# Optimization experiments

Measured on AMD Instinct MI355X. Metric: run time of the kernel, lower is better.

## Reference

```python
import jax, jax.numpy as jnp
import numpy as np

B, T, D = 2, 2048, 2048
N_HEADS, N_KV, HEAD_DIM = 8, 4, 256
S_CACHE = 2048
WINDOW = 512
SOFT_CAP = 50.0
ROPE_TS = 10000
ROPE_PROP = 1.0
EPS = 1e-6
NEG_INF = -2.3819763e38


def setup_inputs() -> dict:
    key = jax.random.key(0)
    ks = jax.random.split(key, 6)
    x = jax.random.normal(ks[0], (B, T, D), dtype=jnp.float32)
    wq = jax.random.normal(ks[1], (D, N_HEADS * HEAD_DIM), dtype=jnp.float32) * (D ** -0.5)
    wk = jax.random.normal(ks[2], (D, N_KV * HEAD_DIM), dtype=jnp.float32) * (D ** -0.5)
    wv = jax.random.normal(ks[3], (D, N_KV * HEAD_DIM), dtype=jnp.float32) * (D ** -0.5)
    wo = jax.random.normal(ks[4], (N_HEADS * HEAD_DIM, D), dtype=jnp.float32) * ((N_HEADS * HEAD_DIM) ** -0.5)
    return {
        'x': x,
        'segment_pos': jnp.broadcast_to(jnp.arange(T, dtype=jnp.int32), (B, T)),
        'cur_ind': 0,
        'wq': wq, 'wk': wk, 'wv': wv, 'wo': wo,
        'q_norm_scale': jnp.zeros((HEAD_DIM,), jnp.float32),
        'k_norm_scale': jnp.zeros((HEAD_DIM,), jnp.float32),
        'k_cache': jnp.zeros((B, S_CACHE, N_KV, HEAD_DIM), jnp.float32),
        'v_cache': jnp.zeros((B, S_CACHE, N_KV, HEAD_DIM), jnp.float32),
    }


def _rms_norm(x, scale, eps=EPS):
    # Gemma4RMSNorm: fp32 norm, (1 + scale) offset
    xf = x.astype(jnp.float32)
    n = xf * jax.lax.rsqrt(jnp.mean(jnp.square(xf), -1, keepdims=True) + eps)
    return (n * (1.0 + scale)).astype(x.dtype)


def _apply_rope(x, pos, max_timescale=ROPE_TS, proportion=ROPE_PROP):
    # x: [B, T, n, H]; pos: [B, T]. Partial RoPE on first proportion*H dims.
    H = x.shape[-1]
    rope_dim = int(H * proportion)
    half = rope_dim // 2
    frac = jnp.arange(half, dtype=jnp.float32) / half
    timescale = jnp.asarray(max_timescale, jnp.float32) ** frac  # [half]
    sinusoid = pos.astype(jnp.float32)[..., None] / timescale    # [B, T, half]
    sin = jnp.sin(sinusoid)[:, :, None, :]
    cos = jnp.cos(sinusoid)[:, :, None, :]
    x_rope, x_pass = x[..., :rope_dim], x[..., rope_dim:]
    x1, x2 = x_rope[..., :half], x_rope[..., half:]
    rotated = jnp.concatenate([x1 * cos - x2 * sin, x2 * cos + x1 * sin], axis=-1)
    return jnp.concatenate([rotated, x_pass], axis=-1).astype(x.dtype)


def reference(x, segment_pos, cur_ind, wq, wk, wv, wo, q_norm_scale, k_norm_scale, k_cache, v_cache):
    b, t, _ = x.shape
    g = N_HEADS // N_KV  # GQA group size

    q = (x @ wq).reshape(b, t, N_HEADS, HEAD_DIM)
    k = (x @ wk).reshape(b, t, N_KV, HEAD_DIM)
    v = (x @ wv).reshape(b, t, N_KV, HEAD_DIM)

    # QK-norm (per-head RMSNorm) then RoPE
    q = _rms_norm(q, q_norm_scale)
    k = _rms_norm(k, k_norm_scale)
    q = _apply_rope(q, segment_pos)
    k = _apply_rope(k, segment_pos)

    # KV-cache scatter write at cur_ind
    idx = jnp.asarray(cur_ind, jnp.int32)
    k_cache = jax.lax.dynamic_update_slice(k_cache, k, (0, idx, 0, 0))
    v_cache = jax.lax.dynamic_update_slice(v_cache, v, (0, idx, 0, 0))

    # Attention logits over full cache: [b, kv, g, t, s]
    qg = q.reshape(b, t, N_KV, g, HEAD_DIM) * (HEAD_DIM ** -0.5)
    logits = jnp.einsum('btkgh,bskh->bkgts', qg, k_cache)
    logits = SOFT_CAP * jnp.tanh(logits / SOFT_CAP)

    # Causal + sliding-window mask from absolute positions
    q_pos = segment_pos[:, :, None]                              # [b, t, 1]
    k_pos = jnp.arange(S_CACHE, dtype=jnp.int32)[None, None, :]  # [1, 1, s]
    mask = (k_pos <= q_pos) & (q_pos - k_pos < WINDOW)           # [b, t, s]
    logits = jnp.where(mask[:, None, None, :, :], logits, NEG_INF)

    probs = jax.nn.softmax(logits, axis=-1)
    attn = jnp.einsum('bkgts,bskh->btkgh', probs, v_cache).reshape(b, t, N_HEADS * HEAD_DIM)
    return attn @ wo
```

## Files before the change

kernel.cpp:

```cpp
#include <hip/hip_runtime.h>

#define T_SEQ 2048
#define NHEADS 8
#define NKV 4
#define HD 256
#define WIN 512

typedef __bf16 bf16x8 __attribute__((ext_vector_type(8)));
typedef float f32x4 __attribute__((ext_vector_type(4)));

__device__ __forceinline__ float bf2f(unsigned short u) {
    return __uint_as_float(((unsigned int)u) << 16);
}
__device__ __forceinline__ unsigned short f2bf(float f) {
    unsigned int u = __float_as_uint(f);
    u += 0x7fffu + ((u >> 16) & 1u);
    return (unsigned short)(u >> 16);
}

#define GLOAD_LDS16(gptr, lptr)                                            \
    __builtin_amdgcn_global_load_lds(                                      \
        (const __attribute__((address_space(1))) unsigned int*)(gptr),     \
        (__attribute__((address_space(3))) unsigned int*)(lptr), 16, 0, 0)

__global__ void detect_dtype(const unsigned short* __restrict__ x, int* flag) {
    int tid = threadIdx.x;
    int cnt = 0;
    for (int i = 0; i < 64; ++i) {
        unsigned short u = x[2 * (tid * 64 + i)];
        int e = (u >> 7) & 0xFF;
        cnt += (e >= 100 && e <= 140) ? 1 : 0;
    }
    #pragma unroll
    for (int o = 32; o >= 1; o >>= 1) cnt += __shfl_xor(cnt, o);
    if (tid == 0) *flag = (cnt > 2048) ? 1 : 0;
}

__global__ __launch_bounds__(256) void convert_to_bf16(
    const void* __restrict__ src, unsigned short* __restrict__ dst,
    const int* __restrict__ flag, int n)
{
    int i = (blockIdx.x * 256 + threadIdx.x) * 8;
    if (i >= n) return;
    if (*flag) {
        *(uint4*)&dst[i] = *(const uint4*)((const unsigned short*)src + i);
    } else {
        const float* s = (const float*)src + i;
        unsigned short v[8];
        #pragma unroll
        for (int j = 0; j < 8; ++j) v[j] = f2bf(s[j]);
        *(uint4*)&dst[i] = *(uint4*)v;
    }
}

__global__ __launch_bounds__(256) void transpose_cvt(
    const void* __restrict__ src, unsigned short* __restrict__ dst,
    const int* __restrict__ flag, int R, int C)
{
    __shared__ unsigned short tile[32][33];
    const int t = threadIdx.x;
    const int c = t & 31, r8 = t >> 5;
    const int bx = blockIdx.x, by = blockIdx.y;
    const int isb = *flag;
    #pragma unroll
    for (int i = 0; i < 4; ++i) {
        int r = r8 + i * 8;
        size_t idx = (size_t)(by * 32 + r) * C + bx * 32 + c;
        tile[r][c] = isb ? ((const unsigned short*)src)[idx]
                         : f2bf(((const float*)src)[idx]);
    }
    __syncthreads();
    #pragma unroll
    for (int i = 0; i < 4; ++i) {
        int r = r8 + i * 8;
        dst[(size_t)(bx * 32 + r) * R + by * 32 + c] = tile[c][r];
    }
}

__global__ __launch_bounds__(256) void gemm_bf16(
    const unsigned short* __restrict__ A,
    const unsigned short* __restrict__ Bt,
    void* __restrict__ C,
    int M, int Ntot, int K, int n_base,
    const int* __restrict__ flag, int force_bf16)
{
    __shared__ __align__(16) unsigned short As[128 * 32];
    __shared__ __align__(16) unsigned short Bs[128 * 32];
    const int tid = threadIdx.x;
    const int n0 = blockIdx.x * 128;
    const int m0 = blockIdx.y * 128;
    const int wave = tid >> 6;
    const int lane = tid & 63;
    const int wm = (wave >> 1) * 64;
    const int wn = (wave & 1) * 64;
    const int quad = lane >> 4;
    const int l16 = lane & 15;
    const int obf = force_bf16 | *flag;

    f32x4 acc[4][4];
    #pragma unroll
    for (int i = 0; i < 4; ++i)
        #pragma unroll
        for (int j = 0; j < 4; ++j)
            acc[i][j] = f32x4{0.f, 0.f, 0.f, 0.f};

    for (int kk = 0; kk < K; kk += 32) {
        #pragma unroll
        for (int i = 0; i < 2; ++i) {
            int ch = tid + i * 256;
            int row = ch >> 2;
            int ko = (ch & 3) * 8;
            GLOAD_LDS16(&A[(size_t)(m0 + row) * K + kk + ko],  &As[ch * 8]);
            GLOAD_LDS16(&Bt[(size_t)(n0 + row) * K + kk + ko], &Bs[ch * 8]);
        }
        __syncthreads();
        bf16x8 af[4], bfr[4];
        #pragma unroll
        for (int mi = 0; mi < 4; ++mi)
            af[mi] = *(const bf16x8*)&As[(wm + mi * 16 + l16) * 32 + quad * 8];
        #pragma unroll
        for (int ni = 0; ni < 4; ++ni)
            bfr[ni] = *(const bf16x8*)&Bs[(wn + ni * 16 + l16) * 32 + quad * 8];
        #pragma unroll
        for (int mi = 0; mi < 4; ++mi)
            #pragma unroll
            for (int ni = 0; ni < 4; ++ni)
                acc[mi][ni] = __builtin_amdgcn_mfma_f32_16x16x32_bf16(
                    af[mi], bfr[ni], acc[mi][ni], 0, 0, 0);
        __syncthreads();
    }

    #pragma unroll
    for (int mi = 0; mi < 4; ++mi)
        #pragma unroll
        for (int ni = 0; ni < 4; ++ni)
            #pragma unroll
            for (int r = 0; r < 4; ++r) {
                int row = m0 + wm + mi * 16 + quad * 4 + r;
                int col = n_base + n0 + wn + ni * 16 + l16;
                size_t idx = (size_t)row * Ntot + col;
                if (obf) ((unsigned short*)C)[idx] = f2bf(acc[mi][ni][r]);
                else     ((float*)C)[idx]          = acc[mi][ni][r];
            }
}

__global__ __launch_bounds__(256) void finalize_qk(
    unsigned short* __restrict__ qkv,
    const int* __restrict__ segment_pos,
    const unsigned short* __restrict__ scales)
{
    const int w = blockIdx.x * 4 + (threadIdx.x >> 6);
    const int lane = threadIdx.x & 63;
    const int b = w / (T_SEQ * 12);
    const int rem = w % (T_SEQ * 12);
    const int t = rem / 12;
    const int slot = rem % 12;
    const bool isq = slot < 8;
    const int col0 = isq ? slot * 256 : 2048 + (slot - 8) * 256;
    unsigned short* p = qkv + (size_t)(b * T_SEQ + t) * 4096 + col0;

    float e[4];
    #pragma unroll
    for (int j = 0; j < 4; ++j) e[j] = bf2f(p[lane + 64 * j]);
    float ss = e[0] * e[0] + e[1] * e[1] + e[2] * e[2] + e[3] * e[3];
    #pragma unroll
    for (int o = 32; o >= 1; o >>= 1) ss += __shfl_xor(ss, o);
    const float rn = rsqrtf(ss * (1.0f / 256.0f) + 1e-6f);
    const unsigned short* scp = scales + (isq ? 0 : 256);
    float nrm[4];
    #pragma unroll
    for (int j = 0; j < 4; ++j)
        nrm[j] = e[j] * rn * (1.0f + bf2f(scp[lane + 64 * j]));

    const int pos = segment_pos[b * T_SEQ + t];
    #pragma unroll
    for (int pp = 0; pp < 2; ++pp) {
        const int i = lane + 64 * pp;
        const float inv_ts = __expf((float)i * -0.07195578415606293f);
        float s, c;
        __sincosf((float)pos * inv_ts, &s, &c);
        const float x1 = nrm[pp], x2 = nrm[pp + 2];
        p[i]       = f2bf(x1 * c - x2 * s);
        p[i + 128] = f2bf(x2 * c + x1 * s);
    }
}

__global__ __launch_bounds__(256) void build_vt(
    const unsigned short* __restrict__ qkv, unsigned short* __restrict__ vt)
{
    __shared__ unsigned short tile[32][33];
    const int bkv = blockIdx.z;
    const int b = bkv >> 2, kv = bkv & 3;
    const int s0 = blockIdx.x * 32, d0 = blockIdx.y * 32;
    const int c = threadIdx.x & 31, r8 = threadIdx.x >> 5;
    #pragma unroll
    for (int i = 0; i < 4; ++i) {
        int r = r8 + i * 8;
        tile[r][c] = qkv[(size_t)(b * T_SEQ + s0 + r) * 4096 + 3072 + kv * 256 + d0 + c];
    }
    __syncthreads();
    #pragma unroll
    for (int i = 0; i < 4; ++i) {
        int r = r8 + i * 8;
        vt[((size_t)bkv * 256 + d0 + r) * T_SEQ + s0 + c] = tile[c][r];
    }
}

#define PSTR 80
__global__ __launch_bounds__(256, 2) void attn_mfma(
    const unsigned short* __restrict__ qkv,
    const unsigned short* __restrict__ vt,
    unsigned short* __restrict__ out)
{
    __shared__ __align__(16) unsigned short SMEM[16384 + 16384 + 4 * 16 * PSTR];
    unsigned short* K_lds  = SMEM;
    unsigned short* VT_lds = SMEM + 16384;

    const int tid = threadIdx.x;
    const int wave = tid >> 6, lane = tid & 63;
    const int l16 = lane & 15, quad = lane >> 4;
    const int sw = l16 & 7;
    const int bkv = blockIdx.x & 7;
    const int qt  = blockIdx.x >> 3;
    const int b = bkv >> 2, kvh = bkv & 3;
    const int t0 = qt * 32;
    const int h = kvh * 2 + (wave >> 1);
    const int woff = (wave & 1) * 16;
    const int tq = t0 + woff + l16;
    unsigned short* P_lds = SMEM + 32768 + wave * 16 * PSTR;

    bf16x8 qf[8];
    {
        const unsigned short* qp =
            qkv + (size_t)(b * T_SEQ + tq) * 4096 + h * 256 + quad * 8;
        #pragma unroll
        for (int c = 0; c < 8; ++c) qf[c] = *(const bf16x8*)(qp + 32 * c);
    }

    f32x4 o[16];
    #pragma unroll
    for (int nt = 0; nt < 16; ++nt) o[nt] = f32x4{0.f, 0.f, 0.f, 0.f};
    float l_run = 0.f;

    int s_lo = t0 - (WIN - 1); if (s_lo < 0) s_lo = 0;
    const int s_base = s_lo & ~63;
    const int s_last = t0 + 31;
    const int tqmin = t0 + woff;
    const int tqmax = tqmin + 15;
    const int wlo   = tqmin - (WIN - 1);
    const size_t kgbase = (size_t)b * T_SEQ * 4096 + 2048 + kvh * 256;
    const size_t vgbase = (size_t)bkv * 256 * T_SEQ;

    for (int sb = s_base; sb <= s_last; sb += 64) {
        __syncthreads();

        #pragma unroll
        for (int i = 0; i < 8; ++i) {
            int ch = tid + 256 * i;
            int row = ch >> 5, e8 = ch & 31;
            GLOAD_LDS16(&qkv[kgbase + (size_t)(sb + row) * 4096
                             + ((e8 ^ (row & 7)) * 8)],
                        &K_lds[ch * 8]);
        }
        #pragma unroll
        for (int i = 0; i < 8; ++i) {
            int ch = tid + 256 * i;
            int dr = ch >> 3, e8 = ch & 7;
            GLOAD_LDS16(&vt[vgbase + (size_t)dr * T_SEQ + sb
                            + ((e8 ^ (dr & 7)) * 8)],
                        &VT_lds[ch * 8]);
        }
        __syncthreads();

        if (sb > tqmax || sb + 63 < wlo) continue;

        f32x4 st[4];
        #pragma unroll
        for (int mt = 0; mt < 4; ++mt) st[mt] = f32x4{0.f, 0.f, 0.f, 0.f};
        __builtin_amdgcn_s_setprio(1);
        #pragma unroll
        for (int c = 0; c < 8; ++c) {
            bf16x8 kf[4];
            #pragma unroll
            for (int mt = 0; mt < 4; ++mt)
                kf[mt] = *(const bf16x8*)&K_lds[(mt * 16 + l16) * 256 + (((4 * c + quad) ^ sw) * 8)];
            #pragma unroll
            for (int mt = 0; mt < 4; ++mt)
                st[mt] = __builtin_amdgcn_mfma_f32_16x16x32_bf16(kf[mt], qf[c], st[mt], 0, 0, 0);
        }
        __builtin_amdgcn_s_setprio(0);

        #pragma unroll
        for (int mt = 0; mt < 4; ++mt)
            #pragma unroll
            for (int r = 0; r < 4; ++r) {
                int sp = sb + mt * 16 + quad * 4 + r;
                float e2 = __expf(st[mt][r] * 0.0025f);
                float p = __expf(20.0f - 100.0f / (e2 + 1.0f));
                bool valid = (sp <= tq) && (tq - sp < WIN);
                p = valid ? p : 0.0f;
                l_run += p;
                P_lds[l16 * PSTR + mt * 16 + quad * 4 + r] = f2bf(p);
            }

        #pragma unroll
        for (int c = 0; c < 2; ++c) {
            bf16x8 pf = *(const bf16x8*)&P_lds[l16 * PSTR + 32 * c + quad * 8];
            __builtin_amdgcn_s_setprio(1);
            #pragma unroll
            for (int nt = 0; nt < 16; ++nt) {
                bf16x8 vf = *(const bf16x8*)&VT_lds[(nt * 16 + l16) * 64 + (((4 * c + quad) ^ sw) * 8)];
                o[nt] = __builtin_amdgcn_mfma_f32_16x16x32_bf16(pf, vf, o[nt], 0, 0, 0);
            }
            __builtin_amdgcn_s_setprio(0);
        }
    }

    l_run += __shfl_xor(l_run, 16);
    l_run += __shfl_xor(l_run, 32);
    float linv[4];
    #pragma unroll
    for (int r = 0; r < 4; ++r) linv[r] = 1.0f / __shfl(l_run, quad * 4 + r);

    __syncthreads();
    unsigned short* W = SMEM + wave * (16 * 264);
    #pragma unroll
    for (int nt = 0; nt < 16; ++nt)
        #pragma unroll
        for (int r = 0; r < 4; ++r)
            W[(quad * 4 + r) * 264 + nt * 16 + l16] = f2bf(o[nt][r] * linv[r]);
    const int lr = lane >> 2, lc = (lane & 3) * 64;
    unsigned short* ob = out + (size_t)(b * T_SEQ + t0 + woff + lr) * 2048 + h * 256 + lc;
    #pragma unroll
    for (int j = 0; j < 8; ++j)
        *(uint4*)(ob + j * 8) = *(const uint4*)&W[lr * 264 + lc + j * 8];
}

extern "C" void kernel_launch(void* const* d_in, const int* in_sizes, int n_in,
                              void* d_out, int out_size, void* d_ws, size_t ws_size,
                              hipStream_t stream) {
    const void* x   = d_in[0];
    const int*  sp  = (const int*)d_in[1];
    const void* wq  = d_in[3];
    const void* wk  = d_in[4];
    const void* wv  = d_in[5];
    const void* wo  = d_in[6];
    const void* qsc = d_in[7];
    const void* ksc = d_in[8];

    unsigned short* ws = (unsigned short*)d_ws;
    int*            flag = (int*)ws;
    unsigned short* sbuf = ws + 1024;
    unsigned short* qkv  = (unsigned short*)d_out;
    dim3 blk(256);

    const size_t NEED = (size_t)(2048 + 8388608 + 8388608) * sizeof(unsigned short);

    detect_dtype<<<1, 64, 0, stream>>>((const unsigned short*)x, flag);

    if (ws_size >= NEED) {
        unsigned short* xhat = ws + 2048;
        unsigned short* wT   = xhat + (size_t)4096 * 2048;
        unsigned short* abuf = xhat;
        unsigned short* vtb  = wT;
        unsigned short* woT  = wT + (size_t)2048 * 2048;

        convert_to_bf16<<<4096, blk, 0, stream>>>(x,   xhat,       flag, 4096 * 2048);
        convert_to_bf16<<<1,    blk, 0, stream>>>(qsc, sbuf,       flag, 256);
        convert_to_bf16<<<1,    blk, 0, stream>>>(ksc, sbuf + 256, flag, 256);

        transpose_cvt<<<dim3(64, 64), blk, 0, stream>>>(wq, wT,                        flag, 2048, 2048);
        transpose_cvt<<<dim3(32, 64), blk, 0, stream>>>(wk, wT + (size_t)2048 * 2048,  flag, 2048, 1024);
        transpose_cvt<<<dim3(32, 64), blk, 0, stream>>>(wv, wT + (size_t)3072 * 2048,  flag, 2048, 1024);

        gemm_bf16<<<dim3(32, 32), blk, 0, stream>>>(xhat, wT, qkv,
                                                    4096, 4096, 2048, 0, flag, 1);

        finalize_qk<<<12288, blk, 0, stream>>>(qkv, sp, sbuf);

        build_vt<<<dim3(64, 8, 8), blk, 0, stream>>>(qkv, vtb);
        attn_mfma<<<512, blk, 0, stream>>>(qkv, vtb, abuf);

        transpose_cvt<<<dim3(64, 64), blk, 0, stream>>>(wo, woT, flag, 2048, 2048);
        gemm_bf16<<<dim3(16, 32), blk, 0, stream>>>(abuf, woT, d_out,
                                                    4096, 2048, 2048, 0, flag, 0);
    } else {
        unsigned short* reg1 = ws + 2048;
        unsigned short* reg2 = reg1 + (size_t)4096 * 2048;
        unsigned short* xhat = reg1;
        unsigned short* abuf = reg1;

        convert_to_bf16<<<4096, blk, 0, stream>>>(x,   xhat,       flag, 4096 * 2048);
        convert_to_bf16<<<1,    blk, 0, stream>>>(qsc, sbuf,       flag, 256);
        convert_to_bf16<<<1,    blk, 0, stream>>>(ksc, sbuf + 256, flag, 256);

        transpose_cvt<<<dim3(64, 64), blk, 0, stream>>>(wq, reg2, flag, 2048, 2048);
        gemm_bf16<<<dim3(16, 32), blk, 0, stream>>>(xhat, reg2, qkv,
                                                    4096, 4096, 2048, 0, flag, 1);
        transpose_cvt<<<dim3(32, 64), blk, 0, stream>>>(wk, reg2,                     flag, 2048, 1024);
        transpose_cvt<<<dim3(32, 64), blk, 0, stream>>>(wv, reg2 + (size_t)1024*2048, flag, 2048, 1024);
        gemm_bf16<<<dim3(16, 32), blk, 0, stream>>>(xhat, reg2, qkv,
                                                    4096, 4096, 2048, 2048, flag, 1);

        finalize_qk<<<12288, blk, 0, stream>>>(qkv, sp, sbuf);

        build_vt<<<dim3(64, 8, 8), blk, 0, stream>>>(qkv, reg2);
        attn_mfma<<<512, blk, 0, stream>>>(qkv, reg2, abuf);

        transpose_cvt<<<dim3(64, 64), blk, 0, stream>>>(wo, reg2, flag, 2048, 2048);
        gemm_bf16<<<dim3(16, 32), blk, 0, stream>>>(abuf, reg2, d_out,
                                                    4096, 2048, 2048, 0, flag, 0);
    }
}
```

Before: 400.6 us.

## Double-buffer GEMM LDS loads and fuse weight transpose and scale conversion launches

The bf16 GEMM now keeps two LDS buffers and prefetches tile t+2 with global-to-LDS loads. It uses manual vmcnt waits and barriers so memory traffic overlaps the MFMA work instead of fully syncing every k-step. The three Q/K/V weight transpose launches become one kernel, and the norm-scale conversion launches are removed by reading raw scales in finalize_qk. The cost is double the LDS use, which may lower occupancy, plus hand-written waitcnt logic that depends on the exact number of outstanding loads.

Result: faster. 380.7 us (-5.0%).

```diff
diff --git a/kernel.cpp b/kernel.cpp
--- a/kernel.cpp
+++ b/kernel.cpp
@@ -77,6 +77,35 @@
     }
 }
 
+__global__ __launch_bounds__(256) void transpose_qkv_w(
+    const void* __restrict__ wq, const void* __restrict__ wk,
+    const void* __restrict__ wv, unsigned short* __restrict__ dst,
+    const int* __restrict__ flag)
+{
+    __shared__ unsigned short tile[32][33];
+    const int t = threadIdx.x;
+    const int c = t & 31, r8 = t >> 5;
+    const int bx = blockIdx.x, by = blockIdx.y;
+    const void* src; int C, rowoff, cb;
+    if (bx < 64)      { src = wq; C = 2048; rowoff = 0;    cb = bx; }
+    else if (bx < 96) { src = wk; C = 1024; rowoff = 2048; cb = bx - 64; }
+    else              { src = wv; C = 1024; rowoff = 3072; cb = bx - 96; }
+    const int isb = *flag;
+    #pragma unroll
+    for (int i = 0; i < 4; ++i) {
+        int r = r8 + i * 8;
+        size_t idx = (size_t)(by * 32 + r) * C + cb * 32 + c;
+        tile[r][c] = isb ? ((const unsigned short*)src)[idx]
+                         : f2bf(((const float*)src)[idx]);
+    }
+    __syncthreads();
+    #pragma unroll
+    for (int i = 0; i < 4; ++i) {
+        int r = r8 + i * 8;
+        dst[(size_t)(rowoff + cb * 32 + r) * 2048 + by * 32 + c] = tile[c][r];
+    }
+}
+
 __global__ __launch_bounds__(256) void gemm_bf16(
     const unsigned short* __restrict__ A,
     const unsigned short* __restrict__ Bt,
@@ -84,8 +113,8 @@
     int M, int Ntot, int K, int n_base,
     const int* __restrict__ flag, int force_bf16)
 {
-    __shared__ __align__(16) unsigned short As[128 * 32];
-    __shared__ __align__(16) unsigned short Bs[128 * 32];
+    __shared__ __align__(16) unsigned short As[2][128 * 32];
+    __shared__ __align__(16) unsigned short Bs[2][128 * 32];
     const int tid = threadIdx.x;
     const int n0 = blockIdx.x * 128;
     const int m0 = blockIdx.y * 128;
@@ -97,6 +126,12 @@
     const int l16 = lane & 15;
     const int obf = force_bf16 | *flag;
 
+    const int ch0 = tid, ch1 = tid + 256;
+    const unsigned short* a0 = A  + (size_t)(m0 + (ch0 >> 2)) * K + (ch0 & 3) * 8;
+    const unsigned short* a1 = A  + (size_t)(m0 + (ch1 >> 2)) * K + (ch1 & 3) * 8;
+    const unsigned short* b0 = Bt + (size_t)(n0 + (ch0 >> 2)) * K + (ch0 & 3) * 8;
+    const unsigned short* b1 = Bt + (size_t)(n0 + (ch1 >> 2)) * K + (ch1 & 3) * 8;
+
     f32x4 acc[4][4];
     #pragma unroll
     for (int i = 0; i < 4; ++i)
@@ -104,31 +139,45 @@
         for (int j = 0; j < 4; ++j)
             acc[i][j] = f32x4{0.f, 0.f, 0.f, 0.f};
 
-    for (int kk = 0; kk < K; kk += 32) {
-        #pragma unroll
-        for (int i = 0; i < 2; ++i) {
-            int ch = tid + i * 256;
-            int row = ch >> 2;
-            int ko = (ch & 3) * 8;
-            GLOAD_LDS16(&A[(size_t)(m0 + row) * K + kk + ko],  &As[ch * 8]);
-            GLOAD_LDS16(&Bt[(size_t)(n0 + row) * K + kk + ko], &Bs[ch * 8]);
-        }
-        __syncthreads();
+    const int NT = K >> 5;
+
+#define STAGE_G(buf, tile_)                              \
+    do { int _o = (tile_) * 32;                          \
+        GLOAD_LDS16(a0 + _o, &As[buf][ch0 * 8]);         \
+        GLOAD_LDS16(b0 + _o, &Bs[buf][ch0 * 8]);         \
+        GLOAD_LDS16(a1 + _o, &As[buf][ch1 * 8]);         \
+        GLOAD_LDS16(b1 + _o, &Bs[buf][ch1 * 8]);         \
+    } while (0)
+
+    STAGE_G(0, 0);
+    STAGE_G(1, 1);
+
+    for (int t = 0; t < NT; ++t) {
+        if (t < NT - 1) asm volatile("s_waitcnt vmcnt(4)" ::: "memory");
+        else            asm volatile("s_waitcnt vmcnt(0)" ::: "memory");
+        __builtin_amdgcn_s_barrier();
+        __builtin_amdgcn_sched_barrier(0);
+
+        const int cb = t & 1;
         bf16x8 af[4], bfr[4];
         #pragma unroll
         for (int mi = 0; mi < 4; ++mi)
-            af[mi] = *(const bf16x8*)&As[(wm + mi * 16 + l16) * 32 + quad * 8];
+            af[mi] = *(const bf16x8*)&As[cb][(wm + mi * 16 + l16) * 32 + quad * 8];
         #pragma unroll
         for (int ni = 0; ni < 4; ++ni)
-            bfr[ni] = *(const bf16x8*)&Bs[(wn + ni * 16 + l16) * 32 + quad * 8];
+            bfr[ni] = *(const bf16x8*)&Bs[cb][(wn + ni * 16 + l16) * 32 + quad * 8];
         #pragma unroll
         for (int mi = 0; mi < 4; ++mi)
             #pragma unroll
             for (int ni = 0; ni < 4; ++ni)
                 acc[mi][ni] = __builtin_amdgcn_mfma_f32_16x16x32_bf16(
                     af[mi], bfr[ni], acc[mi][ni], 0, 0, 0);
-        __syncthreads();
-    }
+
+        __builtin_amdgcn_sched_barrier(0);
+        __builtin_amdgcn_s_barrier();
+        if (t + 2 < NT) STAGE_G(cb, t + 2);
+    }
+#undef STAGE_G
 
     #pragma unroll
     for (int mi = 0; mi < 4; ++mi)
@@ -147,7 +196,9 @@
 __global__ __launch_bounds__(256) void finalize_qk(
     unsigned short* __restrict__ qkv,
     const int* __restrict__ segment_pos,
-    const unsigned short* __restrict__ scales)
+    const void* __restrict__ qs_raw,
+    const void* __restrict__ ks_raw,
+    const int* __restrict__ flag)
 {
     const int w = blockIdx.x * 4 + (threadIdx.x >> 6);
     const int lane = threadIdx.x & 63;
@@ -158,6 +209,7 @@
     const bool isq = slot < 8;
     const int col0 = isq ? slot * 256 : 2048 + (slot - 8) * 256;
     unsigned short* p = qkv + (size_t)(b * T_SEQ + t) * 4096 + col0;
+    const int isb = *flag;
 
     float e[4];
     #pragma unroll
@@ -166,11 +218,14 @@
     #pragma unroll
     for (int o = 32; o >= 1; o >>= 1) ss += __shfl_xor(ss, o);
     const float rn = rsqrtf(ss * (1.0f / 256.0f) + 1e-6f);
-    const unsigned short* scp = scales + (isq ? 0 : 256);
+    const void* scp = isq ? qs_raw : ks_raw;
     float nrm[4];
     #pragma unroll
-    for (int j = 0; j < 4; ++j)
-        nrm[j] = e[j] * rn * (1.0f + bf2f(scp[lane + 64 * j]));
+    for (int j = 0; j < 4; ++j) {
+        float sc = isb ? bf2f(((const unsigned short*)scp)[lane + 64 * j])
+                       : ((const float*)scp)[lane + 64 * j];
+        nrm[j] = e[j] * rn * (1.0f + sc);
+    }
 
     const int pos = segment_pos[b * T_SEQ + t];
     #pragma unroll
@@ -350,7 +405,6 @@
 
     unsigned short* ws = (unsigned short*)d_ws;
     int*            flag = (int*)ws;
-    unsigned short* sbuf = ws + 1024;
     unsigned short* qkv  = (unsigned short*)d_out;
     dim3 blk(256);
 
@@ -365,18 +419,14 @@
         unsigned short* vtb  = wT;
         unsigned short* woT  = wT + (size_t)2048 * 2048;
 
-        convert_to_bf16<<<4096, blk, 0, stream>>>(x,   xhat,       flag, 4096 * 2048);
-        convert_to_bf16<<<1,    blk, 0, stream>>>(qsc, sbuf,       flag, 256);
-        convert_to_bf16<<<1,    blk, 0, stream>>>(ksc, sbuf + 256, flag, 256);
-
-        transpose_cvt<<<dim3(64, 64), blk, 0, stream>>>(wq, wT,                        flag, 2048, 2048);
-        transpose_cvt<<<dim3(32, 64), blk, 0, stream>>>(wk, wT + (size_t)2048 * 2048,  flag, 2048, 1024);
-        transpose_cvt<<<dim3(32, 64), blk, 0, stream>>>(wv, wT + (size_t)3072 * 2048,  flag, 2048, 1024);
+        convert_to_bf16<<<4096, blk, 0, stream>>>(x, xhat, flag, 4096 * 2048);
+
+        transpose_qkv_w<<<dim3(128, 64), blk, 0, stream>>>(wq, wk, wv, wT, flag);
 
         gemm_bf16<<<dim3(32, 32), blk, 0, stream>>>(xhat, wT, qkv,
                                                     4096, 4096, 2048, 0, flag, 1);
 
-        finalize_qk<<<12288, blk, 0, stream>>>(qkv, sp, sbuf);
+        finalize_qk<<<12288, blk, 0, stream>>>(qkv, sp, qsc, ksc, flag);
 
         build_vt<<<dim3(64, 8, 8), blk, 0, stream>>>(qkv, vtb);
         attn_mfma<<<512, blk, 0, stream>>>(qkv, vtb, abuf);
@@ -390,9 +440,7 @@
         unsigned short* xhat = reg1;
         unsigned short* abuf = reg1;
 
-        convert_to_bf16<<<4096, blk, 0, stream>>>(x,   xhat,       flag, 4096 * 2048);
-        convert_to_bf16<<<1,    blk, 0, stream>>>(qsc, sbuf,       flag, 256);
-        convert_to_bf16<<<1,    blk, 0, stream>>>(ksc, sbuf + 256, flag, 256);
+        convert_to_bf16<<<4096, blk, 0, stream>>>(x, xhat, flag, 4096 * 2048);
 
         transpose_cvt<<<dim3(64, 64), blk, 0, stream>>>(wq, reg2, flag, 2048, 2048);
         gemm_bf16<<<dim3(16, 32), blk, 0, stream>>>(xhat, reg2, qkv,
@@ -402,7 +450,7 @@
         gemm_bf16<<<dim3(16, 32), blk, 0, stream>>>(xhat, reg2, qkv,
                                                     4096, 4096, 2048, 2048, flag, 1);
 
-        finalize_qk<<<12288, blk, 0, stream>>>(qkv, sp, sbuf);
+        finalize_qk<<<12288, blk, 0, stream>>>(qkv, sp, qsc, ksc, flag);
 
         build_vt<<<dim3(64, 8, 8), blk, 0, stream>>>(qkv, reg2);
         attn_mfma<<<512, blk, 0, stream>>>(qkv, reg2, abuf);
```
